# Performance work log

Measured on AMD Instinct MI355X. Metric: run time of the kernel, lower is better.

## Reference

```python
import jax, jax.numpy as jnp
import numpy as np

D = 512        # latent_dim
CD = D // 2    # complex_dim = 256
R = 8          # low-rank
UD = 32        # u_dim
NY = 50        # n_y = 2*num_prod + num_inj
SEL_IN = D + UD + 1
H = 128
EPS = 1e-5


def _bn_relu(x, g, b):
    # BatchNorm1d (training mode: batch stats, biased var) + ReLU
    mu = jnp.mean(x, axis=0)
    var = jnp.mean((x - mu) ** 2, axis=0)
    return jax.nn.relu((x - mu) / jnp.sqrt(var + EPS) * g + b)


_LAYERS = [("0", SEL_IN, H), ("1", H, H), ("2", H, D),
           ("a", D, CD), ("o", D, CD),
           ("Ur", D, CD * R), ("Ui", D, CD * R),
           ("Vr", D, CD * R), ("Vi", D, CD * R),
           ("Br", D, CD * UD), ("Bi", D, CD * UD),
           ("Cr", D, NY * CD), ("Ci", D, NY * CD),
           ("D", D, NY * UD)]


def setup_inputs() -> dict:
    key = jax.random.key(0)
    B = 2048
    inp = {}
    k0, k1, k2, kp = jax.random.split(key, 4)
    inp["zt"] = jax.random.normal(k0, (B, D), jnp.float32)
    inp["dt"] = jax.random.uniform(k1, (B, 1), jnp.float32)
    inp["ut"] = jax.random.normal(k2, (B, UD), jnp.float32)
    ks = jax.random.split(kp, len(_LAYERS))
    for (name, fin, fout), k in zip(_LAYERS, ks):
        kw, kb = jax.random.split(k)
        inp["W" + name] = jax.random.normal(kw, (fin, fout), jnp.float32) * 0.02
        inp["b" + name] = jax.random.normal(kb, (fout,), jnp.float32) * 0.02
    # BN affine params for the two hidden selector layers
    inp["g0"] = jnp.ones((H,), jnp.float32)
    inp["be0"] = jnp.zeros((H,), jnp.float32)
    inp["g1"] = jnp.ones((H,), jnp.float32)
    inp["be1"] = jnp.zeros((H,), jnp.float32)
    return inp


def _fwd(zt, dt, ut, W0, b0, g0, be0, W1, b1, g1, be1, W2, b2,
         Wa, ba, Wo, bo, WUr, bUr, WUi, bUi, WVr, bVr, WVi, bVi,
         WBr, bBr, WBi, bBi, WCr, bCr, WCi, bCi, WD, bD):
    B = zt.shape[0]
    z = jax.lax.complex(zt[:, :CD], zt[:, CD:])               # [B, CD] complex
    x = jnp.concatenate([zt, ut, dt], axis=-1)                # [B, SEL_IN]
    h = _bn_relu(x @ W0 + b0, g0, be0)
    h = _bn_relu(h @ W1 + b1, g1, be1)
    hz = h @ W2 + b2                                          # [B, D]

    alpha = -jax.nn.softplus(hz @ Wa + ba)                    # [B, CD]
    omega = hz @ Wo + bo
    Lam = jnp.exp(jax.lax.complex(alpha, omega))              # |Lam| < 1

    U = jax.lax.complex(hz @ WUr + bUr, hz @ WUi + bUi).reshape(B, CD, R)
    V = jax.lax.complex(hz @ WVr + bVr, hz @ WVi + bVi).reshape(B, CD, R)
    # U (V^H z): [B, CD]
    t = jnp.einsum('bdr,bd->br', jnp.conj(V), z)
    low_rank = jnp.einsum('bdr,br->bd', U, t)

    Bt = jax.lax.complex(hz @ WBr + bBr, hz @ WBi + bBi).reshape(B, CD, UD)
    ut_dt = ut * dt                                           # [B, UD] real
    ut_dt_c = ut_dt.astype(Lam.dtype)
    z_next = Lam * z + low_rank + jnp.einsum('bdu,bu->bd', Bt, ut_dt_c)

    Ct = jax.lax.complex(hz @ WCr + bCr, hz @ WCi + bCi).reshape(B, NY, CD)
    Dt = (hz @ WD + bD).reshape(B, NY, UD)
    yt = jnp.einsum('bnd,bd->bn', Ct, z_next).real + jnp.einsum('bnu,bu->bn', Dt, ut_dt)

    z_next_real = jnp.concatenate([z_next.real, z_next.imag], axis=-1)  # [B, D]
    return z_next_real, yt


def reference(zt, dt, ut, W0, b0, g0, be0, W1, b1, g1, be1, W2, b2,
              Wa, ba, Wo, bo, WUr, bUr, WUi, bUi, WVr, bVr, WVi, bVi,
              WBr, bBr, WBi, bBi, WCr, bCr, WCi, bCi, WD, bD):
    return _fwd(zt, dt, ut, W0, b0, g0, be0, W1, b1, g1, be1, W2, b2,
                Wa, ba, Wo, bo, WUr, bUr, WUi, bUi, WVr, bVr, WVi, bVi,
                WBr, bBr, WBi, bBi, WCr, bCr, WCi, bCi, WD, bD)
```

## Files before the change

kernel.cpp:

```cpp
#include <hip/hip_runtime.h>
#include <hip/hip_bf16.h>
#include <cstdint>
#include <cstddef>


typedef __bf16 bf16;
typedef __bf16 bf16x8 __attribute__((ext_vector_type(8)));
typedef float f32x4 __attribute__((ext_vector_type(4)));

__device__ __forceinline__ void async16(const void* g, void* l) {
  __builtin_amdgcn_global_load_lds((const __attribute__((address_space(1))) void*)g,
                                   (__attribute__((address_space(3))) void*)l, 16, 0, 0);
}

__device__ __forceinline__ void gemm_core(const bf16* __restrict__ A,
                                          const bf16* __restrict__ Bw,
                                          int lda, int ldb, int m0, int n0, int K,
                                          bf16* As, bf16* Bs, f32x4 acc[4][4]) {
  const int tid = threadIdx.x;
  const int w = tid >> 6, l = tid & 63;
  const int wm = (w >> 1) << 6, wn = (w & 1) << 6;
  const int fr = l & 15, fk = (l >> 4) << 3;
#pragma unroll
  for (int mt = 0; mt < 4; ++mt)
#pragma unroll
    for (int nt = 0; nt < 4; ++nt) { f32x4 z = {0.f, 0.f, 0.f, 0.f}; acc[mt][nt] = z; }

  for (int kt = 0; kt < K; kt += 32) {
    __syncthreads();
#pragma unroll
    for (int i = 0; i < 2; ++i) {
      int cs = (w << 7) + (i << 6);
      int c = cs + l;
      int row = c >> 2, off = (c & 3) << 3;
      async16(A + (size_t)(m0 + row) * lda + kt + off, As + ((size_t)cs << 3));
      async16(Bw + (size_t)(n0 + row) * ldb + kt + off, Bs + ((size_t)cs << 3));
    }
    __syncthreads();
    bf16x8 af[4], bfr[4];
#pragma unroll
    for (int mt = 0; mt < 4; ++mt) af[mt] = *(const bf16x8*)(As + (wm + mt * 16 + fr) * 32 + fk);
#pragma unroll
    for (int nt = 0; nt < 4; ++nt) bfr[nt] = *(const bf16x8*)(Bs + (wn + nt * 16 + fr) * 32 + fk);
#pragma unroll
    for (int mt = 0; mt < 4; ++mt)
#pragma unroll
      for (int nt = 0; nt < 4; ++nt)
        acc[mt][nt] = __builtin_amdgcn_mfma_f32_16x16x32_bf16(af[mt], bfr[nt], acc[mt][nt], 0, 0, 0);
  }
}

struct TEntry { const float* src; bf16* dst; int K, N, Kpad, tile0, ntn; };
struct TArgs { TEntry e[11]; };

__global__ void k_transpose(TArgs a) {
  __shared__ float tile[64][65];
  int t = blockIdx.x;
  int ei = 0;
  while (ei < 10 && t >= a.e[ei + 1].tile0) ++ei;
  const TEntry E = a.e[ei];
  int lt = t - E.tile0;
  int tk = lt / E.ntn, tn = lt - tk * E.ntn;
  int k0 = tk << 6, n0 = tn << 6;
  int tid = threadIdx.x;
#pragma unroll
  for (int i = 0; i < 16; ++i) {
    int idx = tid + i * 256;
    int kk = idx >> 6, nn = idx & 63;
    int k = k0 + kk, n = n0 + nn;
    tile[nn][kk] = (k < E.K && n < E.N) ? E.src[(size_t)k * E.N + n] : 0.f;
  }
  __syncthreads();
#pragma unroll
  for (int i = 0; i < 16; ++i) {
    int idx = tid + i * 256;
    int nn = idx >> 6, kk = idx & 63;
    int n = n0 + nn, k = k0 + kk;
    if (n < E.N && k < E.Kpad) E.dst[(size_t)n * E.Kpad + k] = (bf16)tile[nn][kk];
  }
}

__global__ void k_prep(const float* ba, const float* bo, const float* bVr, const float* bVi,
                       const float* bBr, const float* bBi, const float* bD,
                       const float* bUr, const float* bUi, const float* bCr, const float* bCi,
                       float* bbigA, float* bbigB, float* bbigC) {
  int i = blockIdx.x * 256 + threadIdx.x;
  if (i < 22656) {
    float v;
    if (i < 256) v = ba[i];
    else if (i < 512) v = bo[i - 256];
    else if (i < 2560) v = bVr[i - 512];
    else if (i < 4608) v = bVi[i - 2560];
    else if (i < 12800) v = bBr[i - 4608];
    else if (i < 20992) v = bBi[i - 12800];
    else if (i < 22592) v = bD[i - 20992];
    else v = 0.f;
    bbigA[i] = v;
  }
  int j = i - 22656;
  if (j >= 0 && j < 4096) bbigB[j] = (j < 2048) ? bUr[j] : bUi[j - 2048];
  int m = i - (22656 + 4096);
  if (m >= 0 && m < 25600) bbigC[m] = (m < 12800) ? bCr[m] : bCi[m - 12800];
}

__global__ void k_lin0(const float* __restrict__ zt, const float* __restrict__ dt,
                       const float* __restrict__ ut, const float* __restrict__ W0,
                       const float* __restrict__ b0, float* __restrict__ s0) {
  int i = blockIdx.x * 256 + threadIdx.x;
  int b = i >> 7, c = i & 127;
  const float* w = W0 + c;
  const float* x = zt + (size_t)b * 512;
  float acc = b0[c];
#pragma unroll 4
  for (int k = 0; k < 512; ++k) acc = fmaf(x[k], w[(size_t)k * 128], acc);
  const float* u = ut + (size_t)b * 32;
#pragma unroll
  for (int k = 0; k < 32; ++k) acc = fmaf(u[k], w[(size_t)(512 + k) * 128], acc);
  acc = fmaf(dt[b], w[(size_t)544 * 128], acc);
  s0[i] = acc;
}

__global__ void k_stats(const float* __restrict__ s, float* __restrict__ mu,
                        float* __restrict__ rstd) {
  int c = blockIdx.x;
  float sm = 0.f, sq = 0.f;
  for (int r = threadIdx.x; r < 2048; r += 256) {
    float v = s[(size_t)r * 128 + c];
    sm += v; sq += v * v;
  }
#pragma unroll
  for (int o = 32; o >= 1; o >>= 1) { sm += __shfl_down(sm, o); sq += __shfl_down(sq, o); }
  __shared__ float red[8];
  int w = threadIdx.x >> 6;
  if ((threadIdx.x & 63) == 0) { red[w] = sm; red[4 + w] = sq; }
  __syncthreads();
  if (threadIdx.x == 0) {
    float S = red[0] + red[1] + red[2] + red[3];
    float Q = red[4] + red[5] + red[6] + red[7];
    float m = S * (1.f / 2048.f);
    float var = Q * (1.f / 2048.f) - m * m;
    mu[c] = m;
    rstd[c] = rsqrtf(var + 1e-5f);
  }
}

__global__ void k_lin1(const float* __restrict__ s0, const float* __restrict__ mu,
                       const float* __restrict__ rstd, const float* __restrict__ g,
                       const float* __restrict__ be, const float* __restrict__ W1,
                       const float* __restrict__ b1, float* __restrict__ s1) {
  int i = blockIdx.x * 256 + threadIdx.x;
  int b = i >> 7, c = i & 127;
  const float* w = W1 + c;
  const float* x = s0 + (size_t)b * 128;
  float acc = b1[c];
#pragma unroll 4
  for (int k = 0; k < 128; ++k) {
    float h = fmaxf(fmaf((x[k] - mu[k]) * rstd[k], g[k], be[k]), 0.f);
    acc = fmaf(h, w[(size_t)k * 128], acc);
  }
  s1[i] = acc;
}

__global__ void k_lin2(const float* __restrict__ s1, const float* __restrict__ mu,
                       const float* __restrict__ rstd, const float* __restrict__ g,
                       const float* __restrict__ be, const float* __restrict__ W2,
                       const float* __restrict__ b2, bf16* __restrict__ hz) {
  int i = blockIdx.x * 256 + threadIdx.x;
  int b = i >> 9, c = i & 511;
  const float* w = W2 + c;
  const float* x = s1 + (size_t)b * 128;
  float acc = b2[c];
#pragma unroll 4
  for (int k = 0; k < 128; ++k) {
    float h = fmaxf(fmaf((x[k] - mu[k]) * rstd[k], g[k], be[k]), 0.f);
    acc = fmaf(h, w[(size_t)k * 512], acc);
  }
  hz[i] = (bf16)acc;
}

__global__ __launch_bounds__(256) void k_gemmA(
    const bf16* __restrict__ hz, const bf16* __restrict__ WT, const float* __restrict__ bias,
    const float* __restrict__ zt, const float* __restrict__ dt, const float* __restrict__ ut,
    float* __restrict__ pa, float* __restrict__ po,
    float* __restrict__ Bzr, float* __restrict__ Bzi,
    float* __restrict__ tbuf, float* __restrict__ ytout) {
  __shared__ __align__(16) bf16 As[4096], Bs[4096];
  f32x4 acc[4][4];
  const int n0 = blockIdx.x * 128, m0 = blockIdx.y * 128;
  gemm_core(hz, WT, 512, 512, m0, n0, 512, As, Bs, acc);
  const int l = threadIdx.x & 63, w = threadIdx.x >> 6;
  const int wm = (w >> 1) << 6, wn = (w & 1) << 6;
  const int fr = l & 15, quad = l >> 4;
  const int ncol = n0 + wn;

  if (n0 < 512) {
    float* dst = (n0 < 256) ? pa : po;
    int cb = ncol - ((n0 < 256) ? 0 : 256);
#pragma unroll
    for (int mt = 0; mt < 4; ++mt)
#pragma unroll
      for (int j = 0; j < 4; ++j) {
        int b = m0 + wm + mt * 16 + quad * 4 + j;
#pragma unroll
        for (int nt = 0; nt < 4; ++nt) {
          int n = ncol + nt * 16 + fr;
          dst[(size_t)b * 256 + (cb + nt * 16 + fr)] = acc[mt][nt][j] + bias[n];
        }
      }
  } else if (n0 < 4608) {
    const bool isVr = n0 < 2560;
#pragma unroll
    for (int mt = 0; mt < 4; ++mt)
#pragma unroll
      for (int j = 0; j < 4; ++j) {
        int b = m0 + wm + mt * 16 + quad * 4 + j;
        float cre = 0.f, cim = 0.f;
#pragma unroll
        for (int nt = 0; nt < 4; ++nt) {
          int n = ncol + nt * 16 + fr;
          float v = acc[mt][nt][j] + bias[n];
          int d = ((n - 512) & 2047) >> 3;
          float zr = zt[(size_t)b * 512 + d], zi = zt[(size_t)b * 512 + 256 + d];
          if (isVr) { cre += v * zr; cim += v * zi; }
          else      { cre += v * zi; cim -= v * zr; }
        }
        cre += __shfl_xor(cre, 8);
        cim += __shfl_xor(cim, 8);
        if ((l & 8) == 0) {
          int r = fr & 7;
          atomicAdd(&tbuf[((size_t)b * 8 + r) * 2 + 0], cre);
          atomicAdd(&tbuf[((size_t)b * 8 + r) * 2 + 1], cim);
        }
      }
  } else if (n0 < 20992) {
    const bool isBr = n0 < 12800;
    float* dst = isBr ? Bzr : Bzi;
#pragma unroll
    for (int mt = 0; mt < 4; ++mt)
#pragma unroll
      for (int j = 0; j < 4; ++j) {
        int b = m0 + wm + mt * 16 + quad * 4 + j;
        float dtb = dt[b];
#pragma unroll
        for (int g = 0; g < 2; ++g) {
          float s = 0.f;
#pragma unroll
          for (int h = 0; h < 2; ++h) {
            int nt = g * 2 + h;
            int n = ncol + nt * 16 + fr;
            int base = (n - 4608) & 8191;
            float v = acc[mt][nt][j] + bias[n];
            s += v * ut[(size_t)b * 32 + (base & 31)];
          }
          s *= dtb;
          s += __shfl_xor(s, 1); s += __shfl_xor(s, 2);
          s += __shfl_xor(s, 4); s += __shfl_xor(s, 8);
          if ((l & 15) == 0) {
            int d = (((ncol + g * 32) - 4608) & 8191) >> 5;
            dst[(size_t)b * 256 + d] = s;
          }
        }
      }
  } else {
#pragma unroll
    for (int mt = 0; mt < 4; ++mt)
#pragma unroll
      for (int j = 0; j < 4; ++j) {
        int b = m0 + wm + mt * 16 + quad * 4 + j;
        float dtb = dt[b];
#pragma unroll
        for (int g = 0; g < 2; ++g) {
          float s = 0.f;
#pragma unroll
          for (int h = 0; h < 2; ++h) {
            int nt = g * 2 + h;
            int n = ncol + nt * 16 + fr;
            int base = n - 20992;
            float v = acc[mt][nt][j] + bias[n];
            s += v * ut[(size_t)b * 32 + (base & 31)];
          }
          s *= dtb;
          s += __shfl_xor(s, 1); s += __shfl_xor(s, 2);
          s += __shfl_xor(s, 4); s += __shfl_xor(s, 8);
          int nn = ((ncol + g * 32) - 20992) >> 5;
          if ((l & 15) == 0 && nn < 50) ytout[(size_t)b * 50 + nn] = s;
        }
      }
  }
}

__global__ __launch_bounds__(256) void k_gemmB(
    const bf16* __restrict__ hz, const bf16* __restrict__ WT, const float* __restrict__ bias,
    const float* __restrict__ tbuf, float* __restrict__ lr) {
  __shared__ __align__(16) bf16 As[4096], Bs[4096];
  f32x4 acc[4][4];
  const int n0 = blockIdx.x * 128, m0 = blockIdx.y * 128;
  gemm_core(hz, WT, 512, 512, m0, n0, 512, As, Bs, acc);
  const int l = threadIdx.x & 63, w = threadIdx.x >> 6;
  const int wm = (w >> 1) << 6, wn = (w & 1) << 6;
  const int fr = l & 15, quad = l >> 4;
  const int ncol = n0 + wn;
  const bool isUr = n0 < 2048;
#pragma unroll
  for (int mt = 0; mt < 4; ++mt)
#pragma unroll
    for (int j = 0; j < 4; ++j) {
      int b = m0 + wm + mt * 16 + quad * 4 + j;
#pragma unroll
      for (int nt = 0; nt < 4; ++nt) {
        int n = ncol + nt * 16 + fr;
        int base = n & 2047;
        int r = base & 7, d = base >> 3;
        float v = acc[mt][nt][j] + bias[n];
        float tre = tbuf[((size_t)b * 8 + r) * 2], tim = tbuf[((size_t)b * 8 + r) * 2 + 1];
        float cre = isUr ? v * tre : -v * tim;
        float cim = isUr ? v * tim :  v * tre;
        cre += __shfl_xor(cre, 1); cre += __shfl_xor(cre, 2); cre += __shfl_xor(cre, 4);
        cim += __shfl_xor(cim, 1); cim += __shfl_xor(cim, 2); cim += __shfl_xor(cim, 4);
        if ((l & 7) == 0) {
          atomicAdd(&lr[((size_t)b * 256 + d) * 2 + 0], cre);
          atomicAdd(&lr[((size_t)b * 256 + d) * 2 + 1], cim);
        }
      }
    }
}

__global__ void k_assembleZ(const float* __restrict__ zt, const float* __restrict__ pa,
                            const float* __restrict__ po, const float* __restrict__ Bzr,
                            const float* __restrict__ Bzi, const float* __restrict__ lr,
                            float* __restrict__ zout, float* __restrict__ znr,
                            float* __restrict__ zni) {
  int i = blockIdx.x * 256 + threadIdx.x;
  int b = i >> 8, d = i & 255;
  float a = pa[i], o = po[i];
  float sp = fmaxf(a, 0.f) + log1pf(expf(-fabsf(a)));
  float mag = expf(-sp);
  float Lr = mag * cosf(o), Li = mag * sinf(o);
  float zr = zt[(size_t)b * 512 + d], zi = zt[(size_t)b * 512 + 256 + d];
  float re = fmaf(Lr, zr, -Li * zi) + Bzr[i] + lr[2 * i];
  float im = fmaf(Lr, zi,  Li * zr) + Bzi[i] + lr[2 * i + 1];
  zout[(size_t)b * 512 + d] = re;
  zout[(size_t)b * 512 + 256 + d] = im;
  znr[i] = re; zni[i] = im;
}

__global__ __launch_bounds__(256) void k_gemmC(
    const bf16* __restrict__ hz, const bf16* __restrict__ WT, const float* __restrict__ bias,
    const float* __restrict__ znr, const float* __restrict__ zni, float* __restrict__ ytout) {
  __shared__ __align__(16) bf16 As[4096], Bs[4096];
  f32x4 acc[4][4];
  const int n0 = blockIdx.x * 128, m0 = blockIdx.y * 128;
  gemm_core(hz, WT, 512, 512, m0, n0, 512, As, Bs, acc);
  const int l = threadIdx.x & 63, w = threadIdx.x >> 6;
  const int wm = (w >> 1) << 6, wn = (w & 1) << 6;
  const int fr = l & 15, quad = l >> 4;
  const int ncol = n0 + wn;
  const bool isCr = n0 < 12800;
  const int nb = ncol - (isCr ? 0 : 12800);
  const int nn = nb >> 8;
#pragma unroll
  for (int mt = 0; mt < 4; ++mt)
#pragma unroll
    for (int j = 0; j < 4; ++j) {
      int b = m0 + wm + mt * 16 + quad * 4 + j;
      float s = 0.f;
#pragma unroll
      for (int nt = 0; nt < 4; ++nt) {
        int n = ncol + nt * 16 + fr;
        int d = (nb + nt * 16 + fr) & 255;
        float v = acc[mt][nt][j] + bias[n];
        s += isCr ? v * znr[(size_t)b * 256 + d] : -(v * zni[(size_t)b * 256 + d]);
      }
      s += __shfl_xor(s, 1); s += __shfl_xor(s, 2);
      s += __shfl_xor(s, 4); s += __shfl_xor(s, 8);
      if ((l & 15) == 0) atomicAdd(&ytout[(size_t)b * 50 + nn], s);
    }
}

extern "C" void kernel_launch(void* const* d_in, const int* in_sizes, int n_in,
                              void* d_out, int out_size, void* d_ws, size_t ws_size,
                              hipStream_t stream) {
  (void)in_sizes; (void)n_in; (void)out_size; (void)ws_size;
  const float* zt  = (const float*)d_in[0];
  const float* dt  = (const float*)d_in[1];
  const float* ut  = (const float*)d_in[2];
  const float* W0  = (const float*)d_in[3];  const float* b0  = (const float*)d_in[4];
  const float* W1  = (const float*)d_in[5];  const float* b1  = (const float*)d_in[6];
  const float* W2  = (const float*)d_in[7];  const float* b2  = (const float*)d_in[8];
  const float* Wa  = (const float*)d_in[9];  const float* ba  = (const float*)d_in[10];
  const float* Wo  = (const float*)d_in[11]; const float* bo  = (const float*)d_in[12];
  const float* WUr = (const float*)d_in[13]; const float* bUr = (const float*)d_in[14];
  const float* WUi = (const float*)d_in[15]; const float* bUi = (const float*)d_in[16];
  const float* WVr = (const float*)d_in[17]; const float* bVr = (const float*)d_in[18];
  const float* WVi = (const float*)d_in[19]; const float* bVi = (const float*)d_in[20];
  const float* WBr = (const float*)d_in[21]; const float* bBr = (const float*)d_in[22];
  const float* WBi = (const float*)d_in[23]; const float* bBi = (const float*)d_in[24];
  const float* WCr = (const float*)d_in[25]; const float* bCr = (const float*)d_in[26];
  const float* WCi = (const float*)d_in[27]; const float* bCi = (const float*)d_in[28];
  const float* WD  = (const float*)d_in[29]; const float* bD  = (const float*)d_in[30];
  const float* g0  = (const float*)d_in[31]; const float* be0 = (const float*)d_in[32];
  const float* g1  = (const float*)d_in[33]; const float* be1 = (const float*)d_in[34];
  (void)be0; (void)be1;

  char* ws = (char*)d_ws;
  bf16*  WTbig = (bf16*)(ws + 0);
  bf16*  WTU   = (bf16*)(ws + 23199744);
  bf16*  WTC   = (bf16*)(ws + 27394048);
  bf16*  hz    = (bf16*)(ws + 53608448);
  float* s0    = (float*)(ws + 55705600);
  float* s1    = (float*)(ws + 56754176);
  float* mu0   = (float*)(ws + 57802752);
  float* rstd0 = mu0 + 128;
  float* mu1   = mu0 + 256;
  float* rstd1 = mu0 + 384;
  float* bbigA = (float*)(ws + 57804800);
  float* bbigB = (float*)(ws + 57895424);
  float* bbigC = (float*)(ws + 57911808);
  float* pa    = (float*)(ws + 58014208);
  float* po    = (float*)(ws + 60111360);
  float* Bzr   = (float*)(ws + 62208512);
  float* Bzi   = (float*)(ws + 64305664);
  float* tbuf  = (float*)(ws + 66402816);
  float* lr    = (float*)(ws + 66533888);
  float* znr   = (float*)(ws + 70728192);
  float* zni   = (float*)(ws + 72825344);
  float* zout  = (float*)d_out;
  float* ytout = zout + 2048 * 512;

  k_prep<<<205, 256, 0, stream>>>(ba, bo, bVr, bVi, bBr, bBi, bD, bUr, bUi, bCr, bCi,
                                  bbigA, bbigB, bbigC);

  TArgs ta; int tile0 = 0; int idx = 0;
  auto add = [&](const float* src, bf16* dst, int K, int N, int Kpad) {
    int ntn = (N + 63) >> 6, ntk = (Kpad + 63) >> 6;
    ta.e[idx].src = src; ta.e[idx].dst = dst; ta.e[idx].K = K; ta.e[idx].N = N;
    ta.e[idx].Kpad = Kpad; ta.e[idx].tile0 = tile0; ta.e[idx].ntn = ntn;
    tile0 += ntn * ntk; ++idx;
  };
  add(Wa,  WTbig + (size_t)0 * 512,     512, 256,   512);
  add(Wo,  WTbig + (size_t)256 * 512,   512, 256,   512);
  add(WVr, WTbig + (size_t)512 * 512,   512, 2048,  512);
  add(WVi, WTbig + (size_t)2560 * 512,  512, 2048,  512);
  add(WBr, WTbig + (size_t)4608 * 512,  512, 8192,  512);
  add(WBi, WTbig + (size_t)12800 * 512, 512, 8192,  512);
  add(WD,  WTbig + (size_t)20992 * 512, 512, 1600,  512);
  add(WUr, WTU,                         512, 2048,  512);
  add(WUi, WTU + (size_t)2048 * 512,    512, 2048,  512);
  add(WCr, WTC,                         512, 12800, 512);
  add(WCi, WTC + (size_t)12800 * 512,   512, 12800, 512);
  k_transpose<<<tile0, 256, 0, stream>>>(ta);

  hipMemsetAsync(tbuf, 0, 131072, stream);
  hipMemsetAsync(lr, 0, 4194304, stream);

  k_lin0<<<1024, 256, 0, stream>>>(zt, dt, ut, W0, b0, s0);
  k_stats<<<128, 256, 0, stream>>>(s0, mu0, rstd0);
  k_lin1<<<1024, 256, 0, stream>>>(s0, mu0, rstd0, g0, be0, W1, b1, s1);
  k_stats<<<128, 256, 0, stream>>>(s1, mu1, rstd1);
  k_lin2<<<4096, 256, 0, stream>>>(s1, mu1, rstd1, g1, be1, W2, b2, hz);

  k_gemmA<<<dim3(177, 16), 256, 0, stream>>>(hz, WTbig, bbigA, zt, dt, ut,
                                             pa, po, Bzr, Bzi, tbuf, ytout);
  k_gemmB<<<dim3(32, 16), 256, 0, stream>>>(hz, WTU, bbigB, tbuf, lr);
  k_assembleZ<<<2048, 256, 0, stream>>>(zt, pa, po, Bzr, Bzi, lr, zout, znr, zni);
  k_gemmC<<<dim3(200, 16), 256, 0, stream>>>(hz, WTC, bbigC, znr, zni, ytout);
}
```

Baseline: 645.5 us.

## Double-buffer GEMM LDS loads with swizzle, grouped tile order, vectorized transpose

```diff
diff --git a/kernel.cpp b/kernel.cpp
--- a/kernel.cpp
+++ b/kernel.cpp
@@ -6,6 +6,7 @@
 
 typedef __bf16 bf16;
 typedef __bf16 bf16x8 __attribute__((ext_vector_type(8)));
+typedef __bf16 bf16x4 __attribute__((ext_vector_type(4)));
 typedef float f32x4 __attribute__((ext_vector_type(4)));
 
 __device__ __forceinline__ void async16(const void* g, void* l) {
@@ -13,44 +14,79 @@
                                    (__attribute__((address_space(3))) void*)l, 16, 0, 0);
 }
 
-__device__ __forceinline__ void gemm_core(const bf16* __restrict__ A,
-                                          const bf16* __restrict__ Bw,
-                                          int lda, int ldb, int m0, int n0, int K,
-                                          bf16* As, bf16* Bs, f32x4 acc[4][4]) {
+__device__ __forceinline__ bool tile_map(int NT, int& m0, int& n0) {
+  int L = blockIdx.x;
+  int x = L & 7, s = L >> 3;
+  int nt = ((s >> 4) << 3) + x;
+  if (nt >= NT) return false;
+  n0 = nt << 7;
+  m0 = (s & 15) << 7;
+  return true;
+}
+
+__device__ __forceinline__ void gemm_core512(const bf16* __restrict__ A,
+                                             const bf16* __restrict__ Bw,
+                                             int m0, int n0,
+                                             bf16* As, bf16* Bs, f32x4 acc[4][4]) {
   const int tid = threadIdx.x;
   const int w = tid >> 6, l = tid & 63;
   const int wm = (w >> 1) << 6, wn = (w & 1) << 6;
-  const int fr = l & 15, fk = (l >> 4) << 3;
+  const int fr = l & 15, quad = l >> 4;
 #pragma unroll
   for (int mt = 0; mt < 4; ++mt)
 #pragma unroll
     for (int nt = 0; nt < 4; ++nt) { f32x4 z = {0.f, 0.f, 0.f, 0.f}; acc[mt][nt] = z; }
 
-  for (int kt = 0; kt < K; kt += 32) {
-    __syncthreads();
-#pragma unroll
-    for (int i = 0; i < 2; ++i) {
-      int cs = (w << 7) + (i << 6);
-      int c = cs + l;
-      int row = c >> 2, off = (c & 3) << 3;
-      async16(A + (size_t)(m0 + row) * lda + kt + off, As + ((size_t)cs << 3));
-      async16(Bw + (size_t)(n0 + row) * ldb + kt + off, Bs + ((size_t)cs << 3));
+  const int c0 = (w << 7) + l, c1 = c0 + 64;
+  const int r0 = c0 >> 2, k0 = ((c0 & 3) ^ ((r0 >> 1) & 3)) << 3;
+  const int r1 = c1 >> 2, k1 = ((c1 & 3) ^ ((r1 >> 1) & 3)) << 3;
+  const bf16* a0 = A + (size_t)(m0 + r0) * 512 + k0;
+  const bf16* a1 = A + (size_t)(m0 + r1) * 512 + k1;
+  const bf16* b0 = Bw + (size_t)(n0 + r0) * 512 + k0;
+  const bf16* b1 = Bw + (size_t)(n0 + r1) * 512 + k1;
+  const int ldsb = w << 10;
+  const int sw8 = (quad ^ ((fr >> 1) & 3)) << 3;
+
+  auto issue = [&](int kt, int p) {
+    bf16* ab = As + p * 4096 + ldsb;
+    bf16* bb = Bs + p * 4096 + ldsb;
+    async16(a0 + kt, ab);
+    async16(a1 + kt, ab + 512);
+    async16(b0 + kt, bb);
+    async16(b1 + kt, bb + 512);
+  };
+
+  issue(0, 0);
+#pragma unroll
+  for (int it = 0; it < 16; ++it) {
+    const int p = it & 1;
+    if (it < 15) {
+      issue((it + 1) << 5, p ^ 1);
+      asm volatile("s_waitcnt vmcnt(4)" ::: "memory");
+    } else {
+      asm volatile("s_waitcnt vmcnt(0)" ::: "memory");
     }
-    __syncthreads();
-    bf16x8 af[4], bfr[4];
-#pragma unroll
-    for (int mt = 0; mt < 4; ++mt) af[mt] = *(const bf16x8*)(As + (wm + mt * 16 + fr) * 32 + fk);
-#pragma unroll
-    for (int nt = 0; nt < 4; ++nt) bfr[nt] = *(const bf16x8*)(Bs + (wn + nt * 16 + fr) * 32 + fk);
+    asm volatile("s_barrier" ::: "memory");
+    const bf16* as = As + p * 4096;
+    const bf16* bs = Bs + p * 4096;
+    bf16x8 af[4], bfv[4];
 #pragma unroll
     for (int mt = 0; mt < 4; ++mt)
+      af[mt] = *(const bf16x8*)(as + (wm + mt * 16 + fr) * 32 + sw8);
+#pragma unroll
+    for (int nt = 0; nt < 4; ++nt)
+      bfv[nt] = *(const bf16x8*)(bs + (wn + nt * 16 + fr) * 32 + sw8);
+    asm volatile("s_waitcnt lgkmcnt(0)" ::: "memory");
+    asm volatile("s_barrier" ::: "memory");
+#pragma unroll
+    for (int mt = 0; mt < 4; ++mt)
 #pragma unroll
       for (int nt = 0; nt < 4; ++nt)
-        acc[mt][nt] = __builtin_amdgcn_mfma_f32_16x16x32_bf16(af[mt], bfr[nt], acc[mt][nt], 0, 0, 0);
-  }
-}
-
-struct TEntry { const float* src; bf16* dst; int K, N, Kpad, tile0, ntn; };
+        acc[mt][nt] = __builtin_amdgcn_mfma_f32_16x16x32_bf16(af[mt], bfv[nt], acc[mt][nt], 0, 0, 0);
+  }
+}
+
+struct TEntry { const float* src; bf16* dst; int N, tile0, ntn; };
 struct TArgs { TEntry e[11]; };
 
 __global__ void k_transpose(TArgs a) {
@@ -64,19 +100,22 @@
   int k0 = tk << 6, n0 = tn << 6;
   int tid = threadIdx.x;
 #pragma unroll
-  for (int i = 0; i < 16; ++i) {
+  for (int i = 0; i < 4; ++i) {
     int idx = tid + i * 256;
-    int kk = idx >> 6, nn = idx & 63;
-    int k = k0 + kk, n = n0 + nn;
-    tile[nn][kk] = (k < E.K && n < E.N) ? E.src[(size_t)k * E.N + n] : 0.f;
+    int kk = idx >> 4, c4 = (idx & 15) << 2;
+    const float4 v = *(const float4*)(E.src + (size_t)(k0 + kk) * E.N + n0 + c4);
+    tile[c4 + 0][kk] = v.x; tile[c4 + 1][kk] = v.y;
+    tile[c4 + 2][kk] = v.z; tile[c4 + 3][kk] = v.w;
   }
   __syncthreads();
 #pragma unroll
-  for (int i = 0; i < 16; ++i) {
+  for (int i = 0; i < 4; ++i) {
     int idx = tid + i * 256;
-    int nn = idx >> 6, kk = idx & 63;
-    int n = n0 + nn, k = k0 + kk;
-    if (n < E.N && k < E.Kpad) E.dst[(size_t)n * E.Kpad + k] = (bf16)tile[nn][kk];
+    int nn = idx >> 4, k4 = (idx & 15) << 2;
+    bf16x4 o;
+    o[0] = (bf16)tile[nn][k4 + 0]; o[1] = (bf16)tile[nn][k4 + 1];
+    o[2] = (bf16)tile[nn][k4 + 2]; o[3] = (bf16)tile[nn][k4 + 3];
+    *(bf16x4*)(E.dst + (size_t)(n0 + nn) * 512 + k0 + k4) = o;
   }
 }
 
@@ -184,10 +223,11 @@
     float* __restrict__ pa, float* __restrict__ po,
     float* __restrict__ Bzr, float* __restrict__ Bzi,
     float* __restrict__ tbuf, float* __restrict__ ytout) {
-  __shared__ __align__(16) bf16 As[4096], Bs[4096];
+  int m0, n0;
+  if (!tile_map(177, m0, n0)) return;
+  __shared__ __align__(16) bf16 As[8192], Bs[8192];
   f32x4 acc[4][4];
-  const int n0 = blockIdx.x * 128, m0 = blockIdx.y * 128;
-  gemm_core(hz, WT, 512, 512, m0, n0, 512, As, Bs, acc);
+  gemm_core512(hz, WT, m0, n0, As, Bs, acc);
   const int l = threadIdx.x & 63, w = threadIdx.x >> 6;
   const int wm = (w >> 1) << 6, wn = (w & 1) << 6;
   const int fr = l & 15, quad = l >> 4;
@@ -292,10 +332,11 @@
 __global__ __launch_bounds__(256) void k_gemmB(
     const bf16* __restrict__ hz, const bf16* __restrict__ WT, const float* __restrict__ bias,
     const float* __restrict__ tbuf, float* __restrict__ lr) {
-  __shared__ __align__(16) bf16 As[4096], Bs[4096];
+  int m0, n0;
+  if (!tile_map(32, m0, n0)) return;
+  __shared__ __align__(16) bf16 As[8192], Bs[8192];
   f32x4 acc[4][4];
-  const int n0 = blockIdx.x * 128, m0 = blockIdx.y * 128;
-  gemm_core(hz, WT, 512, 512, m0, n0, 512, As, Bs, acc);
+  gemm_core512(hz, WT, m0, n0, As, Bs, acc);
   const int l = threadIdx.x & 63, w = threadIdx.x >> 6;
   const int wm = (w >> 1) << 6, wn = (w & 1) << 6;
   const int fr = l & 15, quad = l >> 4;
@@ -347,10 +388,11 @@
 __global__ __launch_bounds__(256) void k_gemmC(
     const bf16* __restrict__ hz, const bf16* __restrict__ WT, const float* __restrict__ bias,
     const float* __restrict__ znr, const float* __restrict__ zni, float* __restrict__ ytout) {
-  __shared__ __align__(16) bf16 As[4096], Bs[4096];
+  int m0, n0;
+  if (!tile_map(200, m0, n0)) return;
+  __shared__ __align__(16) bf16 As[8192], Bs[8192];
   f32x4 acc[4][4];
-  const int n0 = blockIdx.x * 128, m0 = blockIdx.y * 128;
-  gemm_core(hz, WT, 512, 512, m0, n0, 512, As, Bs, acc);
+  gemm_core512(hz, WT, m0, n0, As, Bs, acc);
   const int l = threadIdx.x & 63, w = threadIdx.x >> 6;
   const int wm = (w >> 1) << 6, wn = (w & 1) << 6;
   const int fr = l & 15, quad = l >> 4;
@@ -400,7 +442,6 @@
   const float* WD  = (const float*)d_in[29]; const float* bD  = (const float*)d_in[30];
   const float* g0  = (const float*)d_in[31]; const float* be0 = (const float*)d_in[32];
   const float* g1  = (const float*)d_in[33]; const float* be1 = (const float*)d_in[34];
-  (void)be0; (void)be1;
 
   char* ws = (char*)d_ws;
   bf16*  WTbig = (bf16*)(ws + 0);
@@ -431,23 +472,23 @@
                                   bbigA, bbigB, bbigC);
 
   TArgs ta; int tile0 = 0; int idx = 0;
-  auto add = [&](const float* src, bf16* dst, int K, int N, int Kpad) {
-    int ntn = (N + 63) >> 6, ntk = (Kpad + 63) >> 6;
-    ta.e[idx].src = src; ta.e[idx].dst = dst; ta.e[idx].K = K; ta.e[idx].N = N;
-    ta.e[idx].Kpad = Kpad; ta.e[idx].tile0 = tile0; ta.e[idx].ntn = ntn;
-    tile0 += ntn * ntk; ++idx;
+  auto add = [&](const float* src, bf16* dst, int N) {
+    int ntn = N >> 6;
+    ta.e[idx].src = src; ta.e[idx].dst = dst; ta.e[idx].N = N;
+    ta.e[idx].tile0 = tile0; ta.e[idx].ntn = ntn;
+    tile0 += ntn * 8; ++idx;
   };
-  add(Wa,  WTbig + (size_t)0 * 512,     512, 256,   512);
-  add(Wo,  WTbig + (size_t)256 * 512,   512, 256,   512);
-  add(WVr, WTbig + (size_t)512 * 512,   512, 2048,  512);
-  add(WVi, WTbig + (size_t)2560 * 512,  512, 2048,  512);
-  add(WBr, WTbig + (size_t)4608 * 512,  512, 8192,  512);
-  add(WBi, WTbig + (size_t)12800 * 512, 512, 8192,  512);
-  add(WD,  WTbig + (size_t)20992 * 512, 512, 1600,  512);
-  add(WUr, WTU,                         512, 2048,  512);
-  add(WUi, WTU + (size_t)2048 * 512,    512, 2048,  512);
-  add(WCr, WTC,                         512, 12800, 512);
-  add(WCi, WTC + (size_t)12800 * 512,   512, 12800, 512);
+  add(Wa,  WTbig + (size_t)0 * 512,     256);
+  add(Wo,  WTbig + (size_t)256 * 512,   256);
+  add(WVr, WTbig + (size_t)512 * 512,   2048);
+  add(WVi, WTbig + (size_t)2560 * 512,  2048);
+  add(WBr, WTbig + (size_t)4608 * 512,  8192);
+  add(WBi, WTbig + (size_t)12800 * 512, 8192);
+  add(WD,  WTbig + (size_t)20992 * 512, 1600);
+  add(WUr, WTU,                         2048);
+  add(WUi, WTU + (size_t)2048 * 512,    2048);
+  add(WCr, WTC,                         12800);
+  add(WCi, WTC + (size_t)12800 * 512,   12800);
   k_transpose<<<tile0, 256, 0, stream>>>(ta);
 
   hipMemsetAsync(tbuf, 0, 131072, stream);
@@ -459,9 +500,9 @@
   k_stats<<<128, 256, 0, stream>>>(s1, mu1, rstd1);
   k_lin2<<<4096, 256, 0, stream>>>(s1, mu1, rstd1, g1, be1, W2, b2, hz);
 
-  k_gemmA<<<dim3(177, 16), 256, 0, stream>>>(hz, WTbig, bbigA, zt, dt, ut,
-                                             pa, po, Bzr, Bzi, tbuf, ytout);
-  k_gemmB<<<dim3(32, 16), 256, 0, stream>>>(hz, WTU, bbigB, tbuf, lr);
+  k_gemmA<<<184 * 16, 256, 0, stream>>>(hz, WTbig, bbigA, zt, dt, ut,
+                                        pa, po, Bzr, Bzi, tbuf, ytout);
+  k_gemmB<<<32 * 16, 256, 0, stream>>>(hz, WTU, bbigB, tbuf, lr);
   k_assembleZ<<<2048, 256, 0, stream>>>(zt, pa, po, Bzr, Bzi, lr, zout, znr, zni);
-  k_gemmC<<<dim3(200, 16), 256, 0, stream>>>(hz, WTC, bbigC, znr, zni, ytout);
-}
+  k_gemmC<<<200 * 16, 256, 0, stream>>>(hz, WTC, bbigC, znr, zni, ytout);
+}
```

Result: faster. 615.5 us (-4.6%).
